# Optimization experiments

Hardware: AMD Instinct MI355X
Metric: run time of the kernel (lower is better)

## Reference

```python
import jax, jax.numpy as jnp
import numpy as np

B, N, C, H = 8, 2048, 1024, 16
D = C // H
FOCUSING_FACTOR = 3
KERNEL = 5
EPS_BN = 1e-5


def setup_inputs() -> dict:
    key = jax.random.key(0)
    ks = jax.random.split(key, 6)
    s = lambda k, shape: jax.random.normal(k, shape, dtype=jnp.float32) * 0.02
    return {
        "hidden_states": jax.random.normal(ks[0], (B, N, C), dtype=jnp.float32),
        "bn_gamma": jnp.ones((C,), jnp.float32),
        "bn_beta": jnp.zeros((C,), jnp.float32),
        "W_qkv": s(ks[1], (C, 3 * C)),
        "b_qkv": jnp.zeros((3 * C,), jnp.float32),
        "scale_p": jnp.zeros((1, 1, C), jnp.float32),
        "dwc_w": s(ks[2], (C, 1, KERNEL)),
        "dwc_b": jnp.zeros((C,), jnp.float32),
        "W_proj": s(ks[3], (C, C)),
        "b_proj": jnp.zeros((C,), jnp.float32),
    }


def _focus(t, scale):
    # Focused feature map: relu kernel, scale, then power-3 sharpening with norm restoration
    t = jax.nn.relu(t) + 1e-6
    t = t / scale
    nrm = jnp.linalg.norm(t, axis=-1, keepdims=True)
    t = t ** FOCUSING_FACTOR
    return t / jnp.linalg.norm(t, axis=-1, keepdims=True) * nrm


def reference(hidden_states, bn_gamma, bn_beta, W_qkv, b_qkv, scale_p, dwc_w, dwc_b, W_proj, b_proj):
    x = hidden_states  # (B, N, C)
    # BatchNorm1d in training mode: per-channel stats over batch and sequence
    mean = jnp.mean(x, axis=(0, 1))
    var = jnp.mean((x - mean) ** 2, axis=(0, 1))  # biased, as torch BN uses
    xn = (x - mean) * jax.lax.rsqrt(var + EPS_BN) * bn_gamma + bn_beta

    qkv = xn @ W_qkv + b_qkv
    q, k, v = jnp.split(qkv, 3, axis=-1)
    scale = jax.nn.softplus(scale_p)
    q = _focus(q, scale)
    k = _focus(k, scale)

    heads = lambda t: t.reshape(B, N, H, D).transpose(0, 2, 1, 3)  # (B,H,N,D)
    qh, kh, vh = heads(q), heads(k), heads(v)

    # Linear attention: O(N*D^2) instead of O(N^2*D)
    z = 1.0 / (jnp.einsum('bhnd,bhd->bhn', qh, kh.sum(axis=2)) + 1e-6)
    kv = jnp.einsum('bhnd,bhne->bhde', kh, vh)  # (B,H,D,D)
    o = jnp.einsum('bhnd,bhde->bhne', qh, kv) * z[..., None]
    o = o.transpose(0, 2, 1, 3).reshape(B, N, C)

    # Depthwise conv residual on v over the sequence dim
    vc = v.transpose(0, 2, 1)  # (B,C,N)
    dwc = jax.lax.conv_general_dilated(
        vc, dwc_w, window_strides=(1,), padding=[(KERNEL // 2, KERNEL // 2)],
        dimension_numbers=('NCH', 'OIH', 'NCH'), feature_group_count=C)
    dwc = (dwc + dwc_b[None, :, None]).transpose(0, 2, 1)

    return (o + dwc) @ W_proj + b_proj
```

## Files before the change

kernel.cpp:

```cpp
#include <hip/hip_runtime.h>


#define DEV __device__ __forceinline__

typedef __attribute__((ext_vector_type(8))) short bf16x8;
typedef __attribute__((ext_vector_type(4))) float f32x4;
typedef unsigned short us;

DEV float bf2f(us u) {
  union { unsigned int i; float f; } v; v.i = ((unsigned int)u) << 16; return v.f;
}
DEV us f2bf(float f) {
  union { float f; unsigned int i; } v; v.f = f;
  unsigned int r = v.i + 0x7FFFu + ((v.i >> 16) & 1u);
  return (us)(r >> 16);
}
DEV void glds16(const us* g, us* l) {
  __builtin_amdgcn_global_load_lds((const __attribute__((address_space(1))) unsigned int*)g,
                                   (__attribute__((address_space(3))) unsigned int*)l, 16, 0, 0);
}

__global__ void zero_f32(float* p, int n) {
  int i = blockIdx.x * 256 + threadIdx.x;
  if (i < n) p[i] = 0.f;
}

__global__ __launch_bounds__(256) void bn_stats(const float* __restrict__ x,
                                                float* __restrict__ s_sum, float* __restrict__ s_sq) {
  int t = threadIdx.x;
  int c0 = t * 4;
  size_t row0 = (size_t)blockIdx.x * 64;
  float s[4] = {0.f,0.f,0.f,0.f}, q[4] = {0.f,0.f,0.f,0.f};
  for (int r = 0; r < 64; ++r) {
    f32x4 v = *(const f32x4*)&x[(row0 + r) * 1024 + c0];
    #pragma unroll
    for (int i = 0; i < 4; ++i) { float f = v[i]; s[i] += f; q[i] += f * f; }
  }
  #pragma unroll
  for (int i = 0; i < 4; ++i) { atomicAdd(&s_sum[c0 + i], s[i]); atomicAdd(&s_sq[c0 + i], q[i]); }
}

__global__ void bn_finalize(const float* __restrict__ s_sum, const float* __restrict__ s_sq,
                            const float* __restrict__ gamma, const float* __restrict__ beta,
                            const float* __restrict__ scalep,
                            float* __restrict__ bn_a, float* __restrict__ bn_b, float* __restrict__ invs) {
  int c = threadIdx.x;
  float mean = s_sum[c] * (1.0f / 16384.0f);
  float var  = s_sq[c] * (1.0f / 16384.0f) - mean * mean;
  float a = gamma[c] * rsqrtf(var + 1e-5f);
  bn_a[c] = a;
  bn_b[c] = beta[c] - mean * a;
  float sv = scalep[c];
  float sp = (sv > 20.f) ? sv : log1pf(expf(sv));
  invs[c] = 1.0f / sp;
}

__global__ __launch_bounds__(256) void xn_to_bf16(const float* __restrict__ x,
                                                  const float* __restrict__ bn_a, const float* __restrict__ bn_b,
                                                  us* __restrict__ xn) {
  size_t base = ((size_t)blockIdx.x * 256 + threadIdx.x) * 8;
  int c = (int)(base & 1023);
  f32x4 a0 = *(const f32x4*)&x[base];
  f32x4 a1 = *(const f32x4*)&x[base + 4];
  uint4 o; us* uo = (us*)&o;
  #pragma unroll
  for (int i = 0; i < 4; ++i) uo[i] = f2bf(bn_a[c + i] * a0[i] + bn_b[c + i]);
  #pragma unroll
  for (int i = 0; i < 4; ++i) uo[4 + i] = f2bf(bn_a[c + 4 + i] * a1[i] + bn_b[c + 4 + i]);
  *(uint4*)&xn[base] = o;
}

__global__ __launch_bounds__(256) void transpose_f32_bf16(const float* __restrict__ in,
                                                          us* __restrict__ out, int R, int Cc) {
  __shared__ float tile[64 * 65];
  int tx = blockIdx.x * 64, ty = blockIdx.y * 64;
  int t = threadIdx.x;
  {
    int rr = t >> 4, g = t & 15;
    #pragma unroll
    for (int p = 0; p < 4; ++p) {
      int r = p * 16 + rr;
      f32x4 v = *(const f32x4*)&in[(size_t)(ty + r) * Cc + tx + g * 4];
      #pragma unroll
      for (int i = 0; i < 4; ++i) tile[r * 65 + g * 4 + i] = v[i];
    }
  }
  __syncthreads();
  {
    int rr = t >> 3, g = t & 7;
    #pragma unroll
    for (int p = 0; p < 2; ++p) {
      int nl = p * 32 + rr;
      uint4 v; us* u = (us*)&v;
      #pragma unroll
      for (int j = 0; j < 8; ++j) u[j] = f2bf(tile[(g * 8 + j) * 65 + nl]);
      *(uint4*)&out[(size_t)(tx + nl) * R + ty + g * 8] = v;
    }
  }
}

template <typename OutT>
__global__ __launch_bounds__(256) void gemm_async(const us* __restrict__ A,
                                                  const us* __restrict__ Bt,
                                                  const float* __restrict__ bias,
                                                  OutT* __restrict__ C,
                                                  int M, int N, int K) {
  __shared__ __align__(16) us As[128 * 64];
  __shared__ __align__(16) us Bs[128 * 64];
  int t = threadIdx.x;
  int n0 = blockIdx.x * 128, m0 = blockIdx.y * 128;
  int wid = t >> 6, lane = t & 63;
  int l16 = lane & 15, qd = lane >> 4;
  int wm = (wid & 1) * 64, wn = (wid >> 1) * 64;
  int rr = lane >> 3, gg = (lane & 7) ^ rr;
  const us* gA = A + (size_t)(m0 + wid * 8 + rr) * K + gg * 8;
  const us* gB = Bt + (size_t)(n0 + wid * 8 + rr) * K + gg * 8;
  us* lA = &As[(wid * 8) * 64];
  us* lB = &Bs[(wid * 8) * 64];

  const f32x4 zero4 = {0.f, 0.f, 0.f, 0.f};
  f32x4 acc[4][4];
  #pragma unroll
  for (int i = 0; i < 4; ++i)
    #pragma unroll
    for (int j = 0; j < 4; ++j) acc[i][j] = zero4;

  for (int k0 = 0; k0 < K; k0 += 64) {
    __syncthreads();
    #pragma unroll
    for (int p = 0; p < 4; ++p) {
      glds16(gA + (size_t)p * 32 * K, lA + p * 32 * 64);
      glds16(gB + (size_t)p * 32 * K, lB + p * 32 * 64);
    }
    gA += 64; gB += 64;
    __syncthreads();
    #pragma unroll
    for (int ks = 0; ks < 2; ++ks) {
      bf16x8 af[4], bfr[4];
      #pragma unroll
      for (int i = 0; i < 4; ++i) {
        int ml = wm + i * 16 + l16;
        af[i] = *(const bf16x8*)&As[ml * 64 + (((ks * 4 + qd) ^ (ml & 7)) * 8)];
        int nl = wn + i * 16 + l16;
        bfr[i] = *(const bf16x8*)&Bs[nl * 64 + (((ks * 4 + qd) ^ (nl & 7)) * 8)];
      }
      #pragma unroll
      for (int i = 0; i < 4; ++i)
        #pragma unroll
        for (int j = 0; j < 4; ++j)
          acc[i][j] = __builtin_amdgcn_mfma_f32_16x16x32_bf16(af[i], bfr[j], acc[i][j], 0, 0, 0);
    }
  }
  #pragma unroll
  for (int i = 0; i < 4; ++i) {
    int row = m0 + wm + i * 16 + qd * 4;
    #pragma unroll
    for (int j = 0; j < 4; ++j) {
      int col = n0 + wn + j * 16 + l16;
      float bv = bias[col];
      #pragma unroll
      for (int rrr = 0; rrr < 4; ++rrr) {
        float val = acc[i][j][rrr] + bv;
        if constexpr (sizeof(OutT) == 2)
          ((us*)C)[(size_t)(row + rrr) * N + col] = f2bf(val);
        else
          ((float*)C)[(size_t)(row + rrr) * N + col] = val;
      }
    }
  }
}

__global__ __launch_bounds__(256) void focus_kernel(us* __restrict__ buf,
                                                    const float* __restrict__ invs) {
  int row = blockIdx.x;
  us* p = buf + (size_t)row * 1024;
  int t = threadIdx.x;
  int c0 = t * 4;
  uint2 v = *(uint2*)&p[c0];
  us* u = (us*)&v;
  float ti[4]; float s2 = 0.f, s6 = 0.f;
  #pragma unroll
  for (int i = 0; i < 4; ++i) {
    float f = bf2f(u[i]);
    f = fmaxf(f, 0.f) + 1e-6f;
    f *= invs[c0 + i];
    ti[i] = f;
    float f2 = f * f;
    s2 += f2; s6 += f2 * f2 * f2;
  }
  #pragma unroll
  for (int off = 32; off > 0; off >>= 1) { s2 += __shfl_down(s2, off); s6 += __shfl_down(s6, off); }
  __shared__ float red[8]; __shared__ float bc;
  int wid = t >> 6, lane = t & 63;
  if (lane == 0) { red[wid] = s2; red[4 + wid] = s6; }
  __syncthreads();
  if (t == 0) {
    float a = red[0] + red[1] + red[2] + red[3];
    float b2 = red[4] + red[5] + red[6] + red[7];
    bc = sqrtf(a / b2);
  }
  __syncthreads();
  float factor = bc;
  #pragma unroll
  for (int i = 0; i < 4; ++i) u[i] = f2bf(ti[i] * ti[i] * ti[i] * factor);
  *(uint2*)&p[c0] = v;
}

__global__ __launch_bounds__(256) void attn_stats3(const us* __restrict__ kbuf,
                                                   const us* __restrict__ vbuf,
                                                   float* __restrict__ ksum,
                                                   float* __restrict__ kvpart) {
  int cx = blockIdx.x, h = blockIdx.y, b = blockIdx.z, bh = b * 16 + h;
  int t = threadIdx.x, wid = t >> 6, lane = t & 63;
  int l16 = lane & 15, qd = lane >> 4;
  int wm = (wid & 1) * 32, wn = (wid >> 1) * 32;
  __shared__ __align__(16) us kT[64 * 80];
  __shared__ __align__(16) us vT[64 * 80];
  const f32x4 zero4 = {0.f, 0.f, 0.f, 0.f};
  f32x4 acc[2][2];
  #pragma unroll
  for (int i = 0; i < 2; ++i)
    #pragma unroll
    for (int j = 0; j < 2; ++j) acc[i][j] = zero4;
  float ksacc = 0.f;
  int np = (t & 31) * 2, ch0 = (t >> 5) * 8;

  for (int ck = 0; ck < 4; ++ck) {
    __syncthreads();
    size_t base = ((size_t)b * 2048 + cx * 256 + ck * 64 + np) * 1024 + h * 64 + ch0;
    uint4 k0 = *(const uint4*)&kbuf[base];
    uint4 k1 = *(const uint4*)&kbuf[base + 1024];
    uint4 v0 = *(const uint4*)&vbuf[base];
    uint4 v1 = *(const uint4*)&vbuf[base + 1024];
    us* pk0 = (us*)&k0; us* pk1 = (us*)&k1; us* pv0 = (us*)&v0; us* pv1 = (us*)&v1;
    #pragma unroll
    for (int i = 0; i < 8; ++i) {
      unsigned int pk = (unsigned int)pk0[i] | ((unsigned int)pk1[i] << 16);
      unsigned int pv = (unsigned int)pv0[i] | ((unsigned int)pv1[i] << 16);
      *(unsigned int*)&kT[(ch0 + i) * 80 + np] = pk;
      *(unsigned int*)&vT[(ch0 + i) * 80 + np] = pv;
    }
    __syncthreads();
    if (t < 64) {
      #pragma unroll
      for (int g = 0; g < 8; ++g) {
        bf16x8 kk = *(const bf16x8*)&kT[t * 80 + g * 8];
        #pragma unroll
        for (int j = 0; j < 8; ++j) ksacc += bf2f(((us*)&kk)[j]);
      }
    }
    #pragma unroll
    for (int ks = 0; ks < 2; ++ks) {
      bf16x8 af[2], bfr[2];
      #pragma unroll
      for (int i = 0; i < 2; ++i) {
        af[i]  = *(const bf16x8*)&kT[(wm + i * 16 + l16) * 80 + ks * 32 + qd * 8];
        bfr[i] = *(const bf16x8*)&vT[(wn + i * 16 + l16) * 80 + ks * 32 + qd * 8];
      }
      #pragma unroll
      for (int i = 0; i < 2; ++i)
        #pragma unroll
        for (int j = 0; j < 2; ++j)
          acc[i][j] = __builtin_amdgcn_mfma_f32_16x16x32_bf16(af[i], bfr[j], acc[i][j], 0, 0, 0);
    }
  }
  float* pp = kvpart + ((size_t)cx * 128 + bh) * 4096;
  #pragma unroll
  for (int i = 0; i < 2; ++i) {
    int d = wm + i * 16 + qd * 4;
    #pragma unroll
    for (int j = 0; j < 2; ++j) {
      int e = wn + j * 16 + l16;
      #pragma unroll
      for (int r = 0; r < 4; ++r) pp[(d + r) * 64 + e] = acc[i][j][r];
    }
  }
  if (t < 64) atomicAdd(&ksum[bh * 64 + t], ksacc);
}

__global__ __launch_bounds__(256) void kv_reduce(const float* __restrict__ part, us* __restrict__ kvT) {
  int bh = blockIdx.x;
  int t = threadIdx.x;
  __shared__ float kvl[4096];
  #pragma unroll
  for (int p = 0; p < 16; ++p) {
    int i = p * 256 + t;
    float s = 0.f;
    #pragma unroll
    for (int c = 0; c < 8; ++c) s += part[((size_t)c * 128 + bh) * 4096 + i];
    kvl[i] = s;
  }
  __syncthreads();
  #pragma unroll
  for (int p = 0; p < 2; ++p) {
    int idx = p * 256 + t;
    int e = idx >> 3, d0 = (idx & 7) * 8;
    uint4 o; us* uo = (us*)&o;
    #pragma unroll
    for (int i = 0; i < 8; ++i) uo[i] = f2bf(kvl[(d0 + i) * 64 + e]);
    *(uint4*)&kvT[(size_t)bh * 4096 + e * 64 + d0] = o;
  }
}

__global__ __launch_bounds__(256) void attn_o2(us* __restrict__ qod,
                                               const us* __restrict__ vbuf,
                                               const float* __restrict__ ksum,
                                               const us* __restrict__ kvT,
                                               const float* __restrict__ dwcw,
                                               const float* __restrict__ dwcb) {
  int nt = blockIdx.x, h = blockIdx.y, b = blockIdx.z, bh = b * 16 + h;
  int t = threadIdx.x, wid = t >> 6, lane = t & 63;
  int l16 = lane & 15, qd = lane >> 4;
  __shared__ __align__(16) us qs[128 * 64];
  __shared__ __align__(16) us bs[64 * 64];
  __shared__ __align__(16) us vs[132 * 64];
  __shared__ float zl[128];
  __shared__ float ksl[64];
  __shared__ float wl[64 * 5];
  __shared__ float bl[64];
  int rS = t >> 3, gS = t & 7;
  size_t qbase = ((size_t)b * 2048 + nt * 128) * 1024 + h * 64;
  #pragma unroll
  for (int p = 0; p < 4; ++p) {
    int r = p * 32 + rS;
    uint4 v = *(const uint4*)&qod[qbase + (size_t)r * 1024 + gS * 8];
    *(uint4*)&qs[r * 64 + ((gS ^ (r & 7)) * 8)] = v;
  }
  #pragma unroll
  for (int p = 0; p < 2; ++p) {
    int r = p * 32 + rS;
    uint4 v = *(const uint4*)&kvT[(size_t)bh * 4096 + r * 64 + gS * 8];
    *(uint4*)&bs[r * 64 + ((gS ^ (r & 7)) * 8)] = v;
  }
  int n0 = nt * 128;
  #pragma unroll
  for (int p = 0; p < 5; ++p) {
    int idx = p * 256 + t;
    if (idx < 1056) {
      int r = idx >> 3, g = idx & 7;
      int n = n0 - 2 + r;
      uint4 v = make_uint4(0, 0, 0, 0);
      if (n >= 0 && n < 2048)
        v = *(const uint4*)&vbuf[((size_t)b * 2048 + n) * 1024 + h * 64 + g * 8];
      *(uint4*)&vs[r * 64 + g * 8] = v;
    }
  }
  if (t < 64) {
    ksl[t] = ksum[bh * 64 + t];
    bl[t] = dwcb[h * 64 + t];
    #pragma unroll
    for (int j = 0; j < 5; ++j) wl[t * 5 + j] = dwcw[(h * 64 + t) * 5 + j];
  }
  __syncthreads();
  if (t < 128) {
    float zs = 0.f;
    #pragma unroll
    for (int g = 0; g < 8; ++g) {
      bf16x8 qv = *(const bf16x8*)&qs[t * 64 + ((g ^ (t & 7)) * 8)];
      #pragma unroll
      for (int j = 0; j < 8; ++j) zs += bf2f(((us*)&qv)[j]) * ksl[g * 8 + j];
    }
    zl[t] = 1.f / (zs + 1e-6f);
  }
  __syncthreads();
  const f32x4 zero4 = {0.f, 0.f, 0.f, 0.f};
  f32x4 acc[2][4];
  #pragma unroll
  for (int i = 0; i < 2; ++i)
    #pragma unroll
    for (int j = 0; j < 4; ++j) acc[i][j] = zero4;
  #pragma unroll
  for (int ks = 0; ks < 2; ++ks) {
    bf16x8 af[2], bfr[4];
    #pragma unroll
    for (int i = 0; i < 2; ++i) {
      int ml = (wid * 2 + i) * 16 + l16;
      af[i] = *(const bf16x8*)&qs[ml * 64 + (((ks * 4 + qd) ^ (ml & 7)) * 8)];
    }
    #pragma unroll
    for (int j = 0; j < 4; ++j) {
      int nl = j * 16 + l16;
      bfr[j] = *(const bf16x8*)&bs[nl * 64 + (((ks * 4 + qd) ^ (nl & 7)) * 8)];
    }
    #pragma unroll
    for (int i = 0; i < 2; ++i)
      #pragma unroll
      for (int j = 0; j < 4; ++j)
        acc[i][j] = __builtin_amdgcn_mfma_f32_16x16x32_bf16(af[i], bfr[j], acc[i][j], 0, 0, 0);
  }
  #pragma unroll
  for (int i = 0; i < 2; ++i) {
    int rl0 = (wid * 2 + i) * 16 + qd * 4;
    #pragma unroll
    for (int j = 0; j < 4; ++j) {
      int e = j * 16 + l16;
      float w0 = wl[e * 5], w1 = wl[e * 5 + 1], w2 = wl[e * 5 + 2], w3 = wl[e * 5 + 3], w4 = wl[e * 5 + 4];
      float vv[8];
      #pragma unroll
      for (int m = 0; m < 8; ++m) vv[m] = bf2f(vs[(rl0 + m) * 64 + e]);
      float bb = bl[e];
      #pragma unroll
      for (int r = 0; r < 4; ++r) {
        float dwc = vv[r] * w0 + vv[r + 1] * w1 + vv[r + 2] * w2 + vv[r + 3] * w3 + vv[r + 4] * w4;
        float o = acc[i][j][r] * zl[rl0 + r] + dwc + bb;
        qod[qbase + (size_t)(rl0 + r) * 1024 + e] = f2bf(o);
      }
    }
  }
}

extern "C" void kernel_launch(void* const* d_in, const int* in_sizes, int n_in,
                              void* d_out, int out_size, void* d_ws, size_t ws_size,
                              hipStream_t stream) {
  const float* x      = (const float*)d_in[0];
  const float* gamma  = (const float*)d_in[1];
  const float* beta   = (const float*)d_in[2];
  const float* Wqkv   = (const float*)d_in[3];
  const float* bqkv   = (const float*)d_in[4];
  const float* scalep = (const float*)d_in[5];
  const float* dwcw   = (const float*)d_in[6];
  const float* dwcb   = (const float*)d_in[7];
  const float* Wproj  = (const float*)d_in[8];
  const float* bproj  = (const float*)d_in[9];
  float* out = (float*)d_out;

  float* wsf = (float*)d_ws;
  float* s_sum  = wsf;
  float* s_sq   = wsf + 1024;
  float* ksum   = wsf + 2048;
  float* bn_a   = wsf + 10240;
  float* bn_b   = wsf + 11264;
  float* invs   = wsf + 12288;
  float* kvpart = wsf + 13312;
  us* kvT = (us*)(wsf + 4207616);
  us* wtq = (us*)(wsf + 4469760);
  us* wtp = (us*)(wsf + 6042624);
  us* kq  = (us*)(wsf + 6566912);
  us* vbf = (us*)d_out;
  us* xnb = (us*)d_out + 16777216;

  zero_f32<<<40, 256, 0, stream>>>(wsf, 10240);
  bn_stats<<<256, 256, 0, stream>>>(x, s_sum, s_sq);
  bn_finalize<<<1, 1024, 0, stream>>>(s_sum, s_sq, gamma, beta, scalep, bn_a, bn_b, invs);
  xn_to_bf16<<<8192, 256, 0, stream>>>(x, bn_a, bn_b, xnb);
  transpose_f32_bf16<<<dim3(48, 16), 256, 0, stream>>>(Wqkv, wtq, 1024, 3072);
  transpose_f32_bf16<<<dim3(16, 16), 256, 0, stream>>>(Wproj, wtp, 1024, 1024);

  gemm_async<us><<<dim3(8, 128), 256, 0, stream>>>(xnb, wtq + 1024 * 1024, bqkv + 1024, kq, 16384, 1024, 1024);
  focus_kernel<<<16384, 256, 0, stream>>>(kq, invs);
  gemm_async<us><<<dim3(8, 128), 256, 0, stream>>>(xnb, wtq + 2048 * 1024, bqkv + 2048, vbf, 16384, 1024, 1024);
  attn_stats3<<<dim3(8, 16, 8), 256, 0, stream>>>(kq, vbf, ksum, kvpart);
  kv_reduce<<<128, 256, 0, stream>>>(kvpart, kvT);
  gemm_async<us><<<dim3(8, 128), 256, 0, stream>>>(xnb, wtq, bqkv, kq, 16384, 1024, 1024);
  focus_kernel<<<16384, 256, 0, stream>>>(kq, invs);
  attn_o2<<<dim3(16, 16, 8), 256, 0, stream>>>(kq, vbf, ksum, kvT, dwcw, dwcb);
  gemm_async<float><<<dim3(8, 128), 256, 0, stream>>>(kq, wtp, bproj, out, 16384, 1024, 1024);
}
```

Baseline: 464.5 us.

## Replace GEMM with 256x256-tile 4-stage pipelined kernel and fuse K/V projections

Replaces the 128x128 single-buffered GEMM with a 256x256-tile, 512-thread kernel. It keeps a 4-deep ring of LDS buffers filled by async global-to-LDS loads, gated by explicit vmcnt waits and raw barriers, and raises MFMA issue priority with setprio. The K and V projections become one launch that routes output columns to two buffers, and a swizzled block order is meant to improve L2 reuse. The larger tiles and deeper pipeline aim to hide load latency and cut per-tile overhead. In exchange they use much more LDS and registers, and the kernel hardcodes K=1024.

```diff
diff --git a/kernel.cpp b/kernel.cpp
--- a/kernel.cpp
+++ b/kernel.cpp
@@ -19,6 +19,8 @@
   __builtin_amdgcn_global_load_lds((const __attribute__((address_space(1))) unsigned int*)g,
                                    (__attribute__((address_space(3))) unsigned int*)l, 16, 0, 0);
 }
+
+#define MEMFENCE asm volatile("" ::: "memory")
 
 __global__ void zero_f32(float* p, int n) {
   int i = blockIdx.x * 256 + threadIdx.x;
@@ -100,71 +102,112 @@
 }
 
 template <typename OutT>
-__global__ __launch_bounds__(256) void gemm_async(const us* __restrict__ A,
+__global__ __launch_bounds__(512, 2) void gemm256(const us* __restrict__ A,
                                                   const us* __restrict__ Bt,
                                                   const float* __restrict__ bias,
-                                                  OutT* __restrict__ C,
-                                                  int M, int N, int K) {
-  __shared__ __align__(16) us As[128 * 64];
-  __shared__ __align__(16) us Bs[128 * 64];
+                                                  OutT* __restrict__ Ca,
+                                                  OutT* __restrict__ Cb) {
+  constexpr int GK = 1024;
+  __shared__ __align__(16) us As[4][128 * 64];
+  __shared__ __align__(16) us Bs[4][128 * 64];
   int t = threadIdx.x;
-  int n0 = blockIdx.x * 128, m0 = blockIdx.y * 128;
   int wid = t >> 6, lane = t & 63;
   int l16 = lane & 15, qd = lane >> 4;
-  int wm = (wid & 1) * 64, wn = (wid >> 1) * 64;
-  int rr = lane >> 3, gg = (lane & 7) ^ rr;
-  const us* gA = A + (size_t)(m0 + wid * 8 + rr) * K + gg * 8;
-  const us* gB = Bt + (size_t)(n0 + wid * 8 + rr) * K + gg * 8;
-  us* lA = &As[(wid * 8) * 64];
-  us* lB = &Bs[(wid * 8) * 64];
-
+  int nwx = gridDim.x;
+  int id = blockIdx.y * nwx + blockIdx.x;
+  int nwg = nwx * (int)gridDim.y;
+  int sw = (id & 7) * (nwg >> 3) + (id >> 3);
+  int n0 = (sw % nwx) * 256, m0 = (sw / nwx) * 256;
+
+  int rr = lane >> 3, sl = lane & 7;
+  int lg = sl ^ rr;
+  int grp = lg >> 2, ch = lg & 3;
+  const us* Abase = A + (size_t)(m0 + wid * 8 + rr + 128 * grp) * GK + ch * 8;
+  const us* Bbase = Bt + (size_t)(n0 + wid * 8 + rr + 128 * grp) * GK + ch * 8;
+  us* lA = (us*)&As[0][0] + (wid * 8) * 64;
+  us* lB = (us*)&Bs[0][0] + (wid * 8) * 64;
+
+  int amG = wid & 1;
+  int wn = (wid >> 1) * 64;
+
+  f32x4 acc[8][4];
   const f32x4 zero4 = {0.f, 0.f, 0.f, 0.f};
-  f32x4 acc[4][4];
-  #pragma unroll
-  for (int i = 0; i < 4; ++i)
+  #pragma unroll
+  for (int i = 0; i < 8; ++i)
     #pragma unroll
     for (int j = 0; j < 4; ++j) acc[i][j] = zero4;
 
-  for (int k0 = 0; k0 < K; k0 += 64) {
-    __syncthreads();
-    #pragma unroll
-    for (int p = 0; p < 4; ++p) {
-      glds16(gA + (size_t)p * 32 * K, lA + p * 32 * 64);
-      glds16(gB + (size_t)p * 32 * K, lB + p * 32 * 64);
-    }
-    gA += 64; gB += 64;
-    __syncthreads();
-    #pragma unroll
-    for (int ks = 0; ks < 2; ++ks) {
-      bf16x8 af[4], bfr[4];
-      #pragma unroll
-      for (int i = 0; i < 4; ++i) {
-        int ml = wm + i * 16 + l16;
-        af[i] = *(const bf16x8*)&As[ml * 64 + (((ks * 4 + qd) ^ (ml & 7)) * 8)];
-        int nl = wn + i * 16 + l16;
-        bfr[i] = *(const bf16x8*)&Bs[nl * 64 + (((ks * 4 + qd) ^ (nl & 7)) * 8)];
-      }
-      #pragma unroll
-      for (int i = 0; i < 4; ++i)
-        #pragma unroll
-        for (int j = 0; j < 4; ++j)
-          acc[i][j] = __builtin_amdgcn_mfma_f32_16x16x32_bf16(af[i], bfr[j], acc[i][j], 0, 0, 0);
-    }
-  }
-  #pragma unroll
-  for (int i = 0; i < 4; ++i) {
-    int row = m0 + wm + i * 16 + qd * 4;
+  auto STAGE = [&](int kt) {
+    int b = kt & 3;
+    const us* sa = Abase + kt * 32;
+    const us* sb = Bbase + kt * 32;
+    #pragma unroll
+    for (int p = 0; p < 2; ++p) {
+      glds16(sa + (size_t)p * 64 * GK, lA + b * 8192 + p * 64 * 64);
+      glds16(sb + (size_t)p * 64 * GK, lB + b * 8192 + p * 64 * 64);
+    }
+  };
+
+  auto BODY = [&](int kt) {
+    int b = kt & 3;
+    bf16x8 af[8], bfr[4];
+    #pragma unroll
+    for (int i = 0; i < 8; ++i) {
+      int ra = i * 16 + l16;
+      int ph = (amG * 4 + qd) ^ (l16 & 7);
+      af[i] = *(const bf16x8*)&As[b][ra * 64 + ph * 8];
+    }
     #pragma unroll
     for (int j = 0; j < 4; ++j) {
-      int col = n0 + wn + j * 16 + l16;
-      float bv = bias[col];
-      #pragma unroll
-      for (int rrr = 0; rrr < 4; ++rrr) {
-        float val = acc[i][j][rrr] + bv;
+      int nr = wn + j * 16;
+      int rb = (nr & 127) + l16;
+      int ph = ((nr >> 7) * 4 + qd) ^ (l16 & 7);
+      bfr[j] = *(const bf16x8*)&Bs[b][rb * 64 + ph * 8];
+    }
+    __builtin_amdgcn_s_setprio(1);
+    #pragma unroll
+    for (int i = 0; i < 8; ++i)
+      #pragma unroll
+      for (int j = 0; j < 4; ++j)
+        acc[i][j] = __builtin_amdgcn_mfma_f32_16x16x32_bf16(af[i], bfr[j], acc[i][j], 0, 0, 0);
+    __builtin_amdgcn_s_setprio(0);
+  };
+
+  STAGE(0); STAGE(1); STAGE(2);
+
+  for (int kt = 0; kt < 29; ++kt) {
+    asm volatile("s_waitcnt vmcnt(8)" ::: "memory");
+    MEMFENCE; __builtin_amdgcn_s_barrier(); MEMFENCE;
+    STAGE(kt + 3);
+    BODY(kt);
+  }
+  asm volatile("s_waitcnt vmcnt(8)" ::: "memory");
+  MEMFENCE; __builtin_amdgcn_s_barrier(); MEMFENCE;
+  BODY(29);
+  asm volatile("s_waitcnt vmcnt(4)" ::: "memory");
+  MEMFENCE; __builtin_amdgcn_s_barrier(); MEMFENCE;
+  BODY(30);
+  asm volatile("s_waitcnt vmcnt(0)" ::: "memory");
+  MEMFENCE; __builtin_amdgcn_s_barrier(); MEMFENCE;
+  BODY(31);
+
+  OutT* Cp; int col0;
+  if (n0 < 1024) { Cp = Ca; col0 = n0; } else { Cp = Cb; col0 = n0 - 1024; }
+  #pragma unroll
+  for (int i = 0; i < 8; ++i) {
+    int row = m0 + amG * 128 + i * 16 + qd * 4;
+    #pragma unroll
+    for (int j = 0; j < 4; ++j) {
+      int fc = n0 + wn + j * 16 + l16;
+      float bv = bias[fc];
+      int col = col0 + wn + j * 16 + l16;
+      #pragma unroll
+      for (int r = 0; r < 4; ++r) {
+        float val = acc[i][j][r] + bv;
         if constexpr (sizeof(OutT) == 2)
-          ((us*)C)[(size_t)(row + rrr) * N + col] = f2bf(val);
+          ((us*)Cp)[(size_t)(row + r) * 1024 + col] = f2bf(val);
         else
-          ((float*)C)[(size_t)(row + rrr) * N + col] = val;
+          ((float*)Cp)[(size_t)(row + r) * 1024 + col] = val;
       }
     }
   }
@@ -446,13 +489,12 @@
   transpose_f32_bf16<<<dim3(48, 16), 256, 0, stream>>>(Wqkv, wtq, 1024, 3072);
   transpose_f32_bf16<<<dim3(16, 16), 256, 0, stream>>>(Wproj, wtp, 1024, 1024);
 
-  gemm_async<us><<<dim3(8, 128), 256, 0, stream>>>(xnb, wtq + 1024 * 1024, bqkv + 1024, kq, 16384, 1024, 1024);
+  gemm256<us><<<dim3(8, 64), 512, 0, stream>>>(xnb, wtq + 1024 * 1024, bqkv + 1024, kq, vbf);
   focus_kernel<<<16384, 256, 0, stream>>>(kq, invs);
-  gemm_async<us><<<dim3(8, 128), 256, 0, stream>>>(xnb, wtq + 2048 * 1024, bqkv + 2048, vbf, 16384, 1024, 1024);
   attn_stats3<<<dim3(8, 16, 8), 256, 0, stream>>>(kq, vbf, ksum, kvpart);
   kv_reduce<<<128, 256, 0, stream>>>(kvpart, kvT);
-  gemm_async<us><<<dim3(8, 128), 256, 0, stream>>>(xnb, wtq, bqkv, kq, 16384, 1024, 1024);
+  gemm256<us><<<dim3(4, 64), 512, 0, stream>>>(xnb, wtq, bqkv, kq, kq);
   focus_kernel<<<16384, 256, 0, stream>>>(kq, invs);
   attn_o2<<<dim3(16, 16, 8), 256, 0, stream>>>(kq, vbf, ksum, kvT, dwcw, dwcb);
-  gemm_async<float><<<dim3(8, 128), 256, 0, stream>>>(kq, wtp, bproj, out, 16384, 1024, 1024);
-}
+  gemm256<float><<<dim3(4, 64), 512, 0, stream>>>(kq, wtp, bproj, out, out);
+}
```

New measurement: 424.9 us. -8.5%, faster.
